# Kernel optimization log

Measured on AMD Instinct MI355X. Metric: run time of the kernel, lower is better.

## Reference

```python
import jax, jax.numpy as jnp
import numpy as np

N_NODES = 50000
N_EDGES = 800000
N_GRAPHS = 256
F_IN = 112   # num_features
DIM = 32     # hidden dim of 2nd GIN layer
OUT_DIM = 64 # output_dim
BN_EPS = 1e-5


def setup_inputs() -> dict:
    key = jax.random.key(0)
    ks = jax.random.split(key, 20)
    def w(k, shape, s=0.05):
        return jax.random.normal(k, shape, dtype=jnp.float32) * s
    return {
        "x": jax.random.normal(ks[0], (N_NODES, F_IN), dtype=jnp.float32),
        "src": jax.random.randint(ks[1], (N_EDGES,), 0, N_NODES),
        "dst": jax.random.randint(ks[2], (N_EDGES,), 0, N_NODES),
        "batch": jnp.sort(jax.random.randint(ks[3], (N_NODES,), 0, N_GRAPHS)),
        # GIN layer 1 MLP: Linear(112,112) -> ReLU -> Linear(112,112)
        "g1_w1": w(ks[4], (F_IN, F_IN)), "g1_b1": jnp.zeros((F_IN,), jnp.float32),
        "g1_w2": w(ks[5], (F_IN, F_IN)), "g1_b2": jnp.zeros((F_IN,), jnp.float32),
        "bn1_g": jnp.ones((F_IN,), jnp.float32), "bn1_b": jnp.zeros((F_IN,), jnp.float32),
        # GIN layer 2 MLP: Linear(112,32) -> ReLU -> Linear(32,32)
        "g2_w1": w(ks[6], (F_IN, DIM)), "g2_b1": jnp.zeros((DIM,), jnp.float32),
        "g2_w2": w(ks[7], (DIM, DIM)), "g2_b2": jnp.zeros((DIM,), jnp.float32),
        "bn2_g": jnp.ones((DIM,), jnp.float32), "bn2_b": jnp.zeros((DIM,), jnp.float32),
        # graph-level head
        "fcxd_w": w(ks[8], (DIM, OUT_DIM)), "fcxd_b": jnp.zeros((OUT_DIM,), jnp.float32),
        "fc1_w": w(ks[9], (64, 32)), "fc1_b": jnp.zeros((32,), jnp.float32),
        "fc2_w": w(ks[10], (32, 16)), "fc2_b": jnp.zeros((16,), jnp.float32),
        "fc3_w": w(ks[11], (16, 8)), "fc3_b": jnp.zeros((8,), jnp.float32),
        "fc4_w": w(ks[12], (8, 2)), "fc4_b": jnp.zeros((2,), jnp.float32),
        "fc5_w": w(ks[13], (2, 1)), "fc5_b": jnp.zeros((1,), jnp.float32),
    }


def _batchnorm(h, g, b):
    # training-mode BatchNorm1d: batch statistics over node axis
    m = h.mean(axis=0)
    v = h.var(axis=0)
    return (h - m) * jax.lax.rsqrt(v + BN_EPS) * g + b


def reference(x, src, dst, batch,
              g1_w1, g1_b1, g1_w2, g1_b2, bn1_g, bn1_b,
              g2_w1, g2_b1, g2_w2, g2_b2, bn2_g, bn2_b,
              fcxd_w, fcxd_b, fc1_w, fc1_b, fc2_w, fc2_b,
              fc3_w, fc3_b, fc4_w, fc4_b, fc5_w, fc5_b):
    # --- GIN layer 1: agg = sum_{j in N(i)} x_j ; h = MLP(x + agg) (eps=0) ---
    agg = jax.ops.segment_sum(x[src], dst, num_segments=N_NODES)
    h = x + agg
    h = jnp.maximum(h @ g1_w1 + g1_b1, 0.0) @ g1_w2 + g1_b2
    h = jnp.maximum(h, 0.0)                     # F.relu after conv
    h = _batchnorm(h, bn1_g, bn1_b)
    # --- GIN layer 2 ---
    agg = jax.ops.segment_sum(h[src], dst, num_segments=N_NODES)
    h = h + agg
    h = jnp.maximum(h @ g2_w1 + g2_b1, 0.0) @ g2_w2 + g2_b2
    h = jnp.maximum(h, 0.0)
    h = _batchnorm(h, bn2_g, bn2_b)
    # --- global_add_pool over graph ids ---
    pooled = jax.ops.segment_sum(h, batch, num_segments=N_GRAPHS)  # [G, 32]
    z = jnp.maximum(pooled @ fcxd_w + fcxd_b, 0.0)  # dropout = identity (eval)
    # dense head: NO activations between fc1..fc5 in the original code
    z = z @ fc1_w + fc1_b
    z = z @ fc2_w + fc2_b
    z = z @ fc3_w + fc3_b
    z = z @ fc4_w + fc4_b
    z = z @ fc5_w + fc5_b
    return z  # [N_GRAPHS, 1]
```

## Files before the change

### kernel.cpp

```cpp
#include <hip/hip_runtime.h>
#include <hip/hip_fp16.h>

#define N_NODES 50000
#define N_EDGES 800000
#define N_GRAPHS 256
#define F_IN 112
#define DIM 32
#define BN_EPS 1e-5
#define HROW 128
#define CAP 64
#define CB 391
#define CBCAP 2560
#define CHUNK 8192
#define NPART 98

typedef __attribute__((ext_vector_type(8))) _Float16 half8;
typedef __attribute__((ext_vector_type(4))) float float4v;

__device__ inline unsigned short f2h_u(float f) {
    union { __half h; unsigned short u; } v; v.h = __float2half(f); return v.u;
}
__device__ inline float h2f_u(unsigned short u) {
    union { unsigned short u; __half h; } v; v.u = u; return __half2float(v.h);
}

__device__ inline void w_split_body(const float* __restrict__ W, int K, int N, int Kpad,
                                    unsigned short* __restrict__ hi_t,
                                    unsigned short* __restrict__ lo_t, int idx) {
    if (idx >= N * Kpad) return;
    int n = idx / Kpad, k = idx - n * Kpad;
    float v = (k < K) ? W[(size_t)k * N + n] : 0.f;
    unsigned short h = f2h_u(v);
    hi_t[idx] = h;
    lo_t[idx] = f2h_u(v - h2f_u(h));
}

#define MB_P  NPART
#define MB_XH (MB_P + 3125)
#define MB_W1 (MB_XH + 14)
#define MB_W2 (MB_W1 + 14)
#define MB_W4 (MB_W2 + 1)
#define MB_GB (MB_W4 + 49)
__global__ __launch_bounds__(1024) void build_kernel(
        const int* __restrict__ src, const int* __restrict__ dst,
        int* __restrict__ gcur,
        int* __restrict__ bucket,
        const float* __restrict__ X, __half* __restrict__ Xh,
        const float* __restrict__ g1_w1, unsigned short* w1h, unsigned short* w1l,
        const float* __restrict__ g1_w2, unsigned short* w2h, unsigned short* w2l,
        const float* __restrict__ g2_w2, unsigned short* w4h, unsigned short* w4l,
        const int* __restrict__ batch, int* __restrict__ goff) {
    int b = blockIdx.x;
    int t = threadIdx.x;
    if (b < MB_P) {
        __shared__ int hist[512];
        __shared__ int lofs[512];
        __shared__ int lcur[512];
        __shared__ int gbase[512];
        __shared__ int staging[CHUNK];
        int base = b * CHUNK;
        int total = min(CHUNK, N_EDGES - base);
        for (int i = t; i < 512; i += 1024) hist[i] = 0;
        __syncthreads();
        int d[8], s[8];
#pragma unroll
        for (int j = 0; j < 8; j++) {
            int i = base + j * 1024 + t;
            if (i < N_EDGES) {
                d[j] = __builtin_nontemporal_load(dst + i);
                s[j] = __builtin_nontemporal_load(src + i);
            } else {
                d[j] = -1;
            }
        }
#pragma unroll
        for (int j = 0; j < 8; j++) {
            if (d[j] >= 0) atomicAdd(&hist[d[j] >> 7], 1);
        }
        __syncthreads();
        if (t < 512) lofs[t] = hist[t];
        __syncthreads();
        for (int o = 1; o < 512; o <<= 1) {
            int add = (t < 512 && t >= o) ? lofs[t - o] : 0;
            __syncthreads();
            if (t < 512) lofs[t] += add;
            __syncthreads();
        }
        if (t < CB) {
            gbase[t] = (hist[t] > 0) ? atomicAdd(&gcur[t], hist[t]) : 0;
        }
        if (t < 512) lcur[t] = lofs[t] - hist[t];
        __syncthreads();
#pragma unroll
        for (int j = 0; j < 8; j++) {
            if (d[j] >= 0) {
                int bb = d[j] >> 7;
                int p = atomicAdd(&lcur[bb], 1);
                staging[p] = (d[j] << 16) | s[j];
            }
        }
        __syncthreads();
        for (int p = t; p < total; p += 1024) {
            int e = staging[p];
            int bb = ((unsigned)e >> 16) >> 7;
            int ls = lofs[bb] - hist[bb];
            int di = gbase[bb] + (p - ls);
            if (di < CBCAP) bucket[(size_t)bb * CBCAP + di] = e;
        }
    } else if (b < MB_XH) {
        int idx = (b - MB_P) * 1024 + t;
        if (idx >= N_NODES * (HROW / 2)) return;
        int row = idx / (HROW / 2), c2 = idx - row * (HROW / 2);
        int col = c2 * 2;
        float2 v = make_float2(0.f, 0.f);
        if (col < F_IN) v = *(const float2*)(X + (size_t)row * F_IN + col);
        ((__half2*)Xh)[idx] = __floats2half2_rn(v.x, v.y);
    } else if (b < MB_W1) {
        w_split_body(g1_w1, F_IN, F_IN, 128, w1h, w1l, (b - MB_XH) * 1024 + t);
    } else if (b < MB_W2) {
        w_split_body(g1_w2, F_IN, F_IN, 128, w2h, w2l, (b - MB_W1) * 1024 + t);
    } else if (b < MB_W4) {
        w_split_body(g2_w2, DIM, DIM, 32, w4h, w4l, (b - MB_W2) * 1024 + t);
    } else {
        int i = (b - MB_W4) * 1024 + t;
        if (i >= N_NODES) return;
        int cur = batch[i];
        int prev = (i == 0) ? -1 : batch[i - 1];
        for (int g = prev + 1; g <= cur; g++) goff[g] = i;
        if (i == N_NODES - 1) {
            for (int g = cur + 1; g <= N_GRAPHS; g++) goff[g] = N_NODES;
        }
    }
}

__global__ __launch_bounds__(1024) void bin_build(const int* __restrict__ gcur,
                                                  const int* __restrict__ bucket,
                                                  unsigned short* __restrict__ perm_pad,
                                                  int* __restrict__ deg) {
    __shared__ __align__(16) unsigned short bins[128][CAP];
    __shared__ int lcur[128];
    int b = blockIdx.x, t = threadIdx.x;
    if (t < 128) lcur[t] = 0;
    __syncthreads();
    int count = min(gcur[b], CBCAP);
    for (int i = t; i < count; i += 1024) {
        int e = bucket[(size_t)b * CBCAP + i];
        int l = ((unsigned)e >> 16) & 127;
        int s = e & 0xFFFF;
        int c = atomicAdd(&lcur[l], 1);
        if (c < CAP) bins[l][c] = (unsigned short)s;
    }
    __syncthreads();
    if (t < 128) {
        int node = b * 128 + t;
        if (node < N_NODES) deg[node] = min(lcur[t], CAP);
    }
    for (int i = t; i < 128 * (CAP / 8); i += 1024) {
        int l = i >> 3, q = i & 7;
        int node = b * 128 + l;
        if (node < N_NODES) {
            ((int4*)&perm_pad[(size_t)node * CAP])[q] = ((const int4*)bins[l])[q];
        }
    }
}

__global__ __launch_bounds__(256) void agg_kernel(const float* __restrict__ X,
                                                  const __half* __restrict__ Xh,
                                                  const int* __restrict__ deg_arr,
                                                  const unsigned short* __restrict__ perm_pad,
                                                  __half* __restrict__ out, int M) {
    constexpr int P = F_IN / 2;
    int w = (blockIdx.x * 256 + threadIdx.x) >> 6;
    int lane = threadIdx.x & 63;
    if (w >= M) return;
    int deg = deg_arr[w];
    const unsigned short* pl = perm_pad + (size_t)w * CAP;
    float ax = 0.f, ay = 0.f;
    int e = 0;
    for (; e + 16 <= deg; e += 16) {
        int s[16];
#pragma unroll
        for (int j = 0; j < 16; j++) s[j] = pl[e + j];
        float2 v[16];
#pragma unroll
        for (int j = 0; j < 16; j++)
            v[j] = __half22float2(*(const __half2*)(Xh + (size_t)s[j] * HROW + 2 * lane));
#pragma unroll
        for (int j = 0; j < 16; j++) { ax += v[j].x; ay += v[j].y; }
    }
    for (; e + 4 <= deg; e += 4) {
        int s0 = pl[e], s1 = pl[e + 1], s2 = pl[e + 2], s3 = pl[e + 3];
        float2 v0 = __half22float2(*(const __half2*)(Xh + (size_t)s0 * HROW + 2 * lane));
        float2 v1 = __half22float2(*(const __half2*)(Xh + (size_t)s1 * HROW + 2 * lane));
        float2 v2 = __half22float2(*(const __half2*)(Xh + (size_t)s2 * HROW + 2 * lane));
        float2 v3 = __half22float2(*(const __half2*)(Xh + (size_t)s3 * HROW + 2 * lane));
        ax += (v0.x + v1.x) + (v2.x + v3.x);
        ay += (v0.y + v1.y) + (v2.y + v3.y);
    }
    for (; e < deg; e++) {
        int s = pl[e];
        float2 v = __half22float2(*(const __half2*)(Xh + (size_t)s * HROW + 2 * lane));
        ax += v.x;
        ay += v.y;
    }
    float2 self = make_float2(0.f, 0.f);
    if (lane < P) self = *(const float2*)(X + (size_t)w * F_IN + 2 * lane);
    ((__half2*)(out + (size_t)w * HROW))[lane] = __floats2half2_rn(self.x + ax, self.y + ay);
}

__global__ __launch_bounds__(256) void agg32_kernel(const __half* __restrict__ Y,
                                                    const int* __restrict__ deg_arr,
                                                    const unsigned short* __restrict__ perm_pad,
                                                    const float* __restrict__ c0,
                                                    const float* __restrict__ b1,
                                                    __half* __restrict__ out, int M) {
    int w = (blockIdx.x * 256 + threadIdx.x) >> 6;
    int lane = threadIdx.x & 63;
    if (w >= M) return;
    int f = lane & 15;
    int g = lane >> 4;
    int deg = deg_arr[w];
    const unsigned short* pl = perm_pad + (size_t)w * CAP;
    float ax = 0.f, ay = 0.f;
    int e = g;
    for (; e + 4 < deg; e += 8) {
        int s0 = pl[e], s1 = pl[e + 4];
        float2 v0 = __half22float2(*(const __half2*)(Y + (size_t)s0 * DIM + 2 * f));
        float2 v1 = __half22float2(*(const __half2*)(Y + (size_t)s1 * DIM + 2 * f));
        ax += v0.x + v1.x;
        ay += v0.y + v1.y;
    }
    if (e < deg) {
        int s0 = pl[e];
        float2 v0 = __half22float2(*(const __half2*)(Y + (size_t)s0 * DIM + 2 * f));
        ax += v0.x;
        ay += v0.y;
    }
    ax += __shfl_xor(ax, 16); ax += __shfl_xor(ax, 32);
    ay += __shfl_xor(ay, 16); ay += __shfl_xor(ay, 32);
    if (g == 0) {
        float2 self = __half22float2(*(const __half2*)(Y + (size_t)w * DIM + 2 * f));
        float deg1 = (float)(deg + 1);
        float zx = fmaxf(self.x + ax + deg1 * c0[2 * f] + b1[2 * f], 0.f);
        float zy = fmaxf(self.y + ay + deg1 * c0[2 * f + 1] + b1[2 * f + 1], 0.f);
        ((__half2*)(out + (size_t)w * DIM))[f] = __floats2half2_rn(zx, zy);
    }
}

__global__ __launch_bounds__(256) void w3_fold(const float* __restrict__ W,
                                               const float* __restrict__ s1,
                                               const float* __restrict__ t1,
                                               unsigned short* __restrict__ hi_t,
                                               unsigned short* __restrict__ lo_t,
                                               float* __restrict__ c0) {
    int idx = blockIdx.x * 256 + threadIdx.x;
    if (idx < DIM * 128) {
        int n = idx >> 7, k = idx & 127;
        float v = (k < F_IN) ? s1[k] * W[(size_t)k * DIM + n] : 0.f;
        unsigned short h = f2h_u(v);
        hi_t[idx] = h;
        lo_t[idx] = f2h_u(v - h2f_u(h));
    }
    if (blockIdx.x == 0 && threadIdx.x < DIM) {
        int n = threadIdx.x;
        float acc = 0.f;
        for (int k = 0; k < F_IN; k++) acc += t1[k] * W[(size_t)k * DIM + n];
        c0[n] = acc;
    }
}

__global__ __launch_bounds__(256) void gemm_mlp112(const unsigned short* __restrict__ A,
                                                   const unsigned short* __restrict__ W1h,
                                                   const unsigned short* __restrict__ W1l,
                                                   const float* __restrict__ b1,
                                                   const unsigned short* __restrict__ W2h,
                                                   const unsigned short* __restrict__ W2l,
                                                   const float* __restrict__ b2,
                                                   __half* __restrict__ Ch,
                                                   float* __restrict__ pbuf, int M) {
    constexpr int NT = 7, N = 112, Kpad = 128, TS = 136;
    __shared__ __align__(16) char smem[64 * TS * 2 + 2 * N * 32 * 2 + 64 * 32 * 2];
    unsigned short* T1 = (unsigned short*)smem;
    unsigned short* Wh = (unsigned short*)(smem + 64 * TS * 2);
    unsigned short* Wl = Wh + N * 32;
    unsigned short* Ah = Wl + N * 32;
    float* sls = (float*)Ah;
    int t = threadIdx.x;
    int lane = t & 63, wid = t >> 6;
    int r0 = blockIdx.x * 64;
    int m = lane & 15, quad = lane >> 4;

    for (int i = t; i < 64 * 16; i += 256) {
        T1[(i >> 4) * TS + 112 + (i & 15)] = 0;
    }

    float4v acc[NT];
#pragma unroll
    for (int nt = 0; nt < NT; nt++) acc[nt] = (float4v){0.f, 0.f, 0.f, 0.f};

    for (int c = 0; c < 4; c++) {
        int kc = c * 32;
        {
            int row = t >> 2, seg = t & 3;
            int grow = r0 + row;
            uint4 v = make_uint4(0, 0, 0, 0);
            if (grow < M) v = *(const uint4*)(A + (size_t)grow * HROW + kc + seg * 8);
            *(uint4*)&Ah[row * 32 + seg * 8] = v;
        }
        for (int idx = t; idx < N * 8; idx += 256) {
            int n = idx >> 3, w = idx & 7;
            int gsrc = n * (Kpad / 4) + (kc >> 2) + w;
            ((uint2*)Wh)[idx] = ((const uint2*)W1h)[gsrc];
            ((uint2*)Wl)[idx] = ((const uint2*)W1l)[gsrc];
        }
        __syncthreads();
        half8 a = *(const half8*)&Ah[(wid * 16 + m) * 32 + quad * 8];
#pragma unroll
        for (int nt = 0; nt < NT; nt++) {
            half8 b_h = *(const half8*)&Wh[(nt * 16 + m) * 32 + quad * 8];
            half8 b_l = *(const half8*)&Wl[(nt * 16 + m) * 32 + quad * 8];
            acc[nt] = __builtin_amdgcn_mfma_f32_16x16x32_f16(a, b_h, acc[nt], 0, 0, 0);
            acc[nt] = __builtin_amdgcn_mfma_f32_16x16x32_f16(a, b_l, acc[nt], 0, 0, 0);
        }
        __syncthreads();
    }

#pragma unroll
    for (int nt = 0; nt < NT; nt++) {
        int col = nt * 16 + m;
        float bb = b1[col];
#pragma unroll
        for (int r = 0; r < 4; r++) {
            int row = wid * 16 + quad * 4 + r;
            T1[row * TS + col] = f2h_u(fmaxf(acc[nt][r] + bb, 0.f));
        }
        acc[nt] = (float4v){0.f, 0.f, 0.f, 0.f};
    }
    __syncthreads();

    for (int c = 0; c < 4; c++) {
        int kc = c * 32;
        for (int idx = t; idx < N * 8; idx += 256) {
            int n = idx >> 3, w = idx & 7;
            int gsrc = n * (Kpad / 4) + (kc >> 2) + w;
            ((uint2*)Wh)[idx] = ((const uint2*)W2h)[gsrc];
            ((uint2*)Wl)[idx] = ((const uint2*)W2l)[gsrc];
        }
        __syncthreads();
        half8 a = *(const half8*)&T1[(wid * 16 + m) * TS + kc + quad * 8];
#pragma unroll
        for (int nt = 0; nt < NT; nt++) {
            half8 b_h = *(const half8*)&Wh[(nt * 16 + m) * 32 + quad * 8];
            half8 b_l = *(const half8*)&Wl[(nt * 16 + m) * 32 + quad * 8];
            acc[nt] = __builtin_amdgcn_mfma_f32_16x16x32_f16(a, b_h, acc[nt], 0, 0, 0);
            acc[nt] = __builtin_amdgcn_mfma_f32_16x16x32_f16(a, b_l, acc[nt], 0, 0, 0);
        }
        __syncthreads();
    }

    float st_s[NT], st_q[NT];
#pragma unroll
    for (int nt = 0; nt < NT; nt++) {
        int col = nt * 16 + m;
        float bb = b2[col];
        float s_loc = 0.f, q_loc = 0.f;
#pragma unroll
        for (int r = 0; r < 4; r++) {
            int row = r0 + wid * 16 + quad * 4 + r;
            float v = fmaxf(acc[nt][r] + bb, 0.f);
            if (row < M) {
                Ch[(size_t)row * HROW + col] = __float2half(v);
                s_loc += v;
                q_loc += v * v;
            }
        }
        st_s[nt] = s_loc;
        st_q[nt] = q_loc;
    }
    for (int i = t; i < 64 * 2; i += 256) {
        int row = r0 + (i >> 1), o = (i & 1) * 8;
        if (row < M) *(uint4*)((unsigned short*)Ch + (size_t)row * HROW + 112 + o) = make_uint4(0, 0, 0, 0);
    }
#pragma unroll
    for (int nt = 0; nt < NT; nt++) {
        float s = st_s[nt], q = st_q[nt];
        s += __shfl_xor(s, 16); s += __shfl_xor(s, 32);
        q += __shfl_xor(q, 16); q += __shfl_xor(q, 32);
        if (quad == 0) {
            sls[wid * 2 * N + nt * 16 + m] = s;
            sls[wid * 2 * N + N + nt * 16 + m] = q;
        }
    }
    __syncthreads();
    for (int j = t; j < 2 * N; j += 256) {
        pbuf[(size_t)blockIdx.x * 2 * N + j] = sls[0 * 2 * N + j] + sls[1 * 2 * N + j] +
                                               sls[2 * 2 * N + j] + sls[3 * 2 * N + j];
    }
}

template <int NT, int KC, int AS, bool RELU, int CHS, bool STATS>
__global__ __launch_bounds__(256) void gemm_mfma_h(const unsigned short* __restrict__ A,
                                                   const unsigned short* __restrict__ Whi,
                                                   const unsigned short* __restrict__ Wlo,
                                                   const float* __restrict__ bias,
                                                   float* __restrict__ C,
                                                   __half* __restrict__ Ch,
                                                   float* __restrict__ pbuf, int M) {
    constexpr int N = NT * 16;
    constexpr int Kpad = KC * 32;
    __shared__ __align__(16) unsigned short Ah[64 * 32];
    __shared__ __align__(16) unsigned short Wh[N * 32];
    __shared__ __align__(16) unsigned short Wl[N * 32];
    int t = threadIdx.x;
    int lane = t & 63, wid = t >> 6;
    int r0 = blockIdx.x * 64;
    int m = lane & 15, quad = lane >> 4;

    float4v acc[NT];
#pragma unroll
    for (int nt = 0; nt < NT; nt++) acc[nt] = (float4v){0.f, 0.f, 0.f, 0.f};

    for (int c = 0; c < KC; c++) {
        int kc = c * 32;
        {
            int row = t >> 2, seg = t & 3;
            int grow = r0 + row;
            uint4 v = make_uint4(0, 0, 0, 0);
            if (grow < M) v = *(const uint4*)(A + (size_t)grow * AS + kc + seg * 8);
            *(uint4*)&Ah[row * 32 + seg * 8] = v;
        }
        for (int idx = t; idx < N * 8; idx += 256) {
            int n = idx >> 3, w = idx & 7;
            int gsrc = n * (Kpad / 4) + (kc >> 2) + w;
            ((uint2*)Wh)[idx] = ((const uint2*)Whi)[gsrc];
            ((uint2*)Wl)[idx] = ((const uint2*)Wlo)[gsrc];
        }
        __syncthreads();
        half8 a = *(const half8*)&Ah[(wid * 16 + m) * 32 + quad * 8];
#pragma unroll
        for (int nt = 0; nt < NT; nt++) {
            half8 b_h = *(const half8*)&Wh[(nt * 16 + m) * 32 + quad * 8];
            half8 b_l = *(const half8*)&Wl[(nt * 16 + m) * 32 + quad * 8];
            acc[nt] = __builtin_amdgcn_mfma_f32_16x16x32_f16(a, b_h, acc[nt], 0, 0, 0);
            acc[nt] = __builtin_amdgcn_mfma_f32_16x16x32_f16(a, b_l, acc[nt], 0, 0, 0);
        }
        __syncthreads();
    }
    float st_s[NT], st_q[NT];
#pragma unroll
    for (int nt = 0; nt < NT; nt++) {
        int col = nt * 16 + m;
        float b = bias ? bias[col] : 0.f;
        float s_loc = 0.f, q_loc = 0.f;
#pragma unroll
        for (int r = 0; r < 4; r++) {
            int row = r0 + wid * 16 + quad * 4 + r;
            float v = acc[nt][r] + b;
            if (RELU) v = fmaxf(v, 0.f);
            if (row < M) {
                if (C) C[(size_t)row * N + col] = v;
                if (Ch) Ch[(size_t)row * CHS + col] = __float2half(v);
                if (STATS) { s_loc += v; q_loc += v * v; }
            }
        }
        st_s[nt] = s_loc;
        st_q[nt] = q_loc;
    }
    if constexpr (STATS) {
        __shared__ float sls[4][2 * N];
#pragma unroll
        for (int nt = 0; nt < NT; nt++) {
            float s = st_s[nt], q = st_q[nt];
            s += __shfl_xor(s, 16); s += __shfl_xor(s, 32);
            q += __shfl_xor(q, 16); q += __shfl_xor(q, 32);
            if (quad == 0) {
                sls[wid][nt * 16 + m] = s;
                sls[wid][N + nt * 16 + m] = q;
            }
        }
        __syncthreads();
        for (int j = t; j < 2 * N; j += 256) {
            pbuf[(size_t)blockIdx.x * 2 * N + j] = sls[0][j] + sls[1][j] + sls[2][j] + sls[3][j];
        }
    }
}

template <int F, int BLOCKS>
__global__ __launch_bounds__(256) void bn_finalize_par(const float* __restrict__ pbuf,
                                                       const float* __restrict__ g,
                                                       const float* __restrict__ b,
                                                       float* __restrict__ s,
                                                       float* __restrict__ tt, int M) {
    __shared__ double red[256];
    int j = blockIdx.x;
    int t = threadIdx.x;
    double sum = 0.0, sq = 0.0;
    for (int i = t; i < BLOCKS; i += 256) {
        sum += (double)pbuf[(size_t)i * 2 * F + j];
        sq  += (double)pbuf[(size_t)i * 2 * F + F + j];
    }
    red[t] = sum;
    __syncthreads();
    for (int o = 128; o > 0; o >>= 1) { if (t < o) red[t] += red[t + o]; __syncthreads(); }
    double total_sum = red[0];
    __syncthreads();
    red[t] = sq;
    __syncthreads();
    for (int o = 128; o > 0; o >>= 1) { if (t < o) red[t] += red[t + o]; __syncthreads(); }
    if (t == 0) {
        double mean = total_sum / M;
        double var = red[0] / M - mean * mean;
        double sc = (double)g[j] / sqrt(var + BN_EPS);
        s[j] = (float)sc;
        tt[j] = (float)((double)b[j] - mean * sc);
    }
}

__global__ __launch_bounds__(256) void pool_head(const float* __restrict__ H2, const int* __restrict__ goff,
                                                 const float* __restrict__ s2, const float* __restrict__ t2,
                                                 const float* __restrict__ fcxd_w, const float* __restrict__ fcxd_b,
                                                 const float* __restrict__ fc1_w, const float* __restrict__ fc1_b,
                                                 const float* __restrict__ fc2_w, const float* __restrict__ fc2_b,
                                                 const float* __restrict__ fc3_w, const float* __restrict__ fc3_b,
                                                 const float* __restrict__ fc4_w, const float* __restrict__ fc4_b,
                                                 const float* __restrict__ fc5_w, const float* __restrict__ fc5_b,
                                                 float* __restrict__ out) {
    __shared__ float red[256];
    __shared__ float p[64];
    __shared__ float z[64];
    int g = blockIdx.x, t = threadIdx.x;
    int r0 = goff[g], r1 = goff[g + 1];
    int cnt = r1 - r0;
    int j = t & 31, rr = t >> 5;
    float a = 0.f;
    for (int r = r0 + rr; r < r1; r += 8) a += H2[(size_t)r * DIM + j];
    red[t] = a;
    __syncthreads();
    if (t < 32) {
        float ssum = 0.f;
        for (int q = 0; q < 8; q++) ssum += red[q * 32 + j];
        p[j] = s2[j] * ssum + (float)cnt * t2[j];
    }
    __syncthreads();
    if (t < 64) {
        float acc = fcxd_b[t];
        for (int i = 0; i < 32; i++) acc += p[i] * fcxd_w[i * 64 + t];
        z[t] = fmaxf(acc, 0.f);
    }
    __syncthreads();
    if (t < 32) {
        float acc = fc1_b[t];
        for (int i = 0; i < 64; i++) acc += z[i] * fc1_w[i * 32 + t];
        p[t] = acc;
    }
    __syncthreads();
    if (t < 16) {
        float acc = fc2_b[t];
        for (int i = 0; i < 32; i++) acc += p[i] * fc2_w[i * 16 + t];
        z[t] = acc;
    }
    __syncthreads();
    if (t < 8) {
        float acc = fc3_b[t];
        for (int i = 0; i < 16; i++) acc += z[i] * fc3_w[i * 8 + t];
        p[t] = acc;
    }
    __syncthreads();
    if (t < 2) {
        float acc = fc4_b[t];
        for (int i = 0; i < 8; i++) acc += p[i] * fc4_w[i * 2 + t];
        z[t] = acc;
    }
    __syncthreads();
    if (t == 0) {
        out[g] = z[0] * fc5_w[0] + z[1] * fc5_w[1] + fc5_b[0];
    }
}

extern "C" void kernel_launch(void* const* d_in, const int* in_sizes, int n_in,
                              void* d_out, int out_size, void* d_ws, size_t ws_size,
                              hipStream_t stream) {
    const float* x     = (const float*)d_in[0];
    const int*   src   = (const int*)d_in[1];
    const int*   dst   = (const int*)d_in[2];
    const int*   batch = (const int*)d_in[3];
    const float* g1_w1 = (const float*)d_in[4];
    const float* g1_b1 = (const float*)d_in[5];
    const float* g1_w2 = (const float*)d_in[6];
    const float* g1_b2 = (const float*)d_in[7];
    const float* bn1_g = (const float*)d_in[8];
    const float* bn1_b = (const float*)d_in[9];
    const float* g2_w1 = (const float*)d_in[10];
    const float* g2_b1 = (const float*)d_in[11];
    const float* g2_w2 = (const float*)d_in[12];
    const float* g2_b2 = (const float*)d_in[13];
    const float* bn2_g = (const float*)d_in[14];
    const float* bn2_b = (const float*)d_in[15];
    const float* fcxd_w = (const float*)d_in[16];
    const float* fcxd_b = (const float*)d_in[17];
    const float* fc1_w = (const float*)d_in[18];
    const float* fc1_b = (const float*)d_in[19];
    const float* fc2_w = (const float*)d_in[20];
    const float* fc2_b = (const float*)d_in[21];
    const float* fc3_w = (const float*)d_in[22];
    const float* fc3_b = (const float*)d_in[23];
    const float* fc4_w = (const float*)d_in[24];
    const float* fc4_b = (const float*)d_in[25];
    const float* fc5_w = (const float*)d_in[26];
    const float* fc5_b = (const float*)d_in[27];
    float* out = (float*)d_out;
    char* ws = (char*)d_ws;

    const int GEMM_MB = (N_NODES + 63) / 64;

    size_t off = 0;
    auto take = [&](size_t bytes) { size_t o = off; off += (bytes + 255) & ~(size_t)255; return o; };
    int* gcur      = (int*)(ws + take((size_t)CB * 4));
    size_t zero_bytes = off;
    int* bucket    = (int*)(ws + take((size_t)CB * CBCAP * 4));
    unsigned short* perm_pad = (unsigned short*)(ws + take((size_t)N_NODES * CAP * 2));
    int* deg       = (int*)(ws + take((size_t)N_NODES * 4));
    int* goff      = (int*)(ws + take((size_t)(N_GRAPHS + 4) * 4));
    float* s1      = (float*)(ws + take(F_IN * 4));
    float* t1      = (float*)(ws + take(F_IN * 4));
    float* s2      = (float*)(ws + take(DIM * 4));
    float* t2      = (float*)(ws + take(DIM * 4));
    float* c0      = (float*)(ws + take(DIM * 4));
    float* pb1     = (float*)(ws + take((size_t)GEMM_MB * 2 * F_IN * 4));
    float* pb2     = (float*)(ws + take((size_t)GEMM_MB * 2 * DIM * 4));
    unsigned short* w1h = (unsigned short*)(ws + take((size_t)F_IN * 128 * 2));
    unsigned short* w1l = (unsigned short*)(ws + take((size_t)F_IN * 128 * 2));
    unsigned short* w2h = (unsigned short*)(ws + take((size_t)F_IN * 128 * 2));
    unsigned short* w2l = (unsigned short*)(ws + take((size_t)F_IN * 128 * 2));
    unsigned short* w3h = (unsigned short*)(ws + take((size_t)DIM * 128 * 2));
    unsigned short* w3l = (unsigned short*)(ws + take((size_t)DIM * 128 * 2));
    unsigned short* w4h = (unsigned short*)(ws + take((size_t)DIM * 32 * 2));
    unsigned short* w4l = (unsigned short*)(ws + take((size_t)DIM * 32 * 2));
    __half* x_half = (__half*)(ws + take((size_t)N_NODES * HROW * 2));
    __half* aggA   = (__half*)(ws + take((size_t)N_NODES * HROW * 2));
    __half* h1h    = (__half*)(ws + take((size_t)N_NODES * HROW * 2));
    __half* y_half = (__half*)(ws + take((size_t)N_NODES * DIM * 2));
    __half* s1h    = (__half*)(ws + take((size_t)N_NODES * DIM * 2));
    float* bufS2   = (float*)(ws + take((size_t)N_NODES * DIM * 4));
    (void)ws_size; (void)in_sizes; (void)n_in; (void)out_size;

    hipMemsetAsync(ws, 0, zero_bytes, stream);

    build_kernel<<<MB_GB, 1024, 0, stream>>>(src, dst, gcur, bucket,
                                             x, x_half,
                                             g1_w1, w1h, w1l, g1_w2, w2h, w2l, g2_w2, w4h, w4l,
                                             batch, goff);
    bin_build<<<CB, 1024, 0, stream>>>(gcur, bucket, perm_pad, deg);

    const int AGG_BLOCKS = (N_NODES + 3) / 4;

    agg_kernel<<<AGG_BLOCKS, 256, 0, stream>>>(x, x_half, deg, perm_pad, aggA, N_NODES);
    gemm_mlp112<<<GEMM_MB, 256, 0, stream>>>((const unsigned short*)aggA, w1h, w1l, g1_b1,
                                             w2h, w2l, g1_b2, h1h, pb1, N_NODES);
    bn_finalize_par<F_IN, 782><<<F_IN, 256, 0, stream>>>(pb1, bn1_g, bn1_b, s1, t1, N_NODES);

    w3_fold<<<(DIM * 128 + 255) / 256, 256, 0, stream>>>(g2_w1, s1, t1, w3h, w3l, c0);
    gemm_mfma_h<2, 4, HROW, false, DIM, false><<<GEMM_MB, 256, 0, stream>>>(
        (const unsigned short*)h1h, w3h, w3l, nullptr, nullptr, y_half, nullptr, N_NODES);
    agg32_kernel<<<AGG_BLOCKS, 256, 0, stream>>>(y_half, deg, perm_pad, c0, g2_b1, s1h, N_NODES);
    gemm_mfma_h<2, 1, DIM, true, 0, true><<<GEMM_MB, 256, 0, stream>>>(
        (const unsigned short*)s1h, w4h, w4l, g2_b2, bufS2, nullptr, pb2, N_NODES);
    bn_finalize_par<DIM, 782><<<DIM, 256, 0, stream>>>(pb2, bn2_g, bn2_b, s2, t2, N_NODES);

    pool_head<<<N_GRAPHS, 256, 0, stream>>>(bufS2, goff, s2, t2,
                                            fcxd_w, fcxd_b, fc1_w, fc1_b, fc2_w, fc2_b,
                                            fc3_w, fc3_b, fc4_w, fc4_b, fc5_w, fc5_b, out);
}
```

Baseline: 244.9 us.

## Fuse neighbor aggregation into GIN MLP GEMMs and merge BN1 finalize with W3 fold

The layer-1 gather-sum is folded into the MLP GEMM kernel, which now writes the aggregated tile straight into shared memory instead of a global fp16 buffer. The layer-2 aggregation and ReLU are likewise fused with the second small GEMM and its BN statistics. The BN1 finalize and the W3 scale/fold are merged into one kernel that updates c0 with atomics, and c0/w3 are added to the zeroed workspace region. This drops two intermediate global round-trips and several launches. The cost is that the gather phase now runs at GEMM-grid occupancy, with 64 rows per block and higher shared-memory use, which may hide latency less well than the old standalone aggregation kernels.

```diff
diff --git a/kernel.cpp b/kernel.cpp
--- a/kernel.cpp
+++ b/kernel.cpp
@@ -13,6 +13,7 @@
 #define CBCAP 2560
 #define CHUNK 8192
 #define NPART 98
+#define GEMM_MB 782
 
 typedef __attribute__((ext_vector_type(8))) _Float16 half8;
 typedef __attribute__((ext_vector_type(4))) float float4v;
@@ -164,132 +165,75 @@
     }
 }
 
-__global__ __launch_bounds__(256) void agg_kernel(const float* __restrict__ X,
-                                                  const __half* __restrict__ Xh,
-                                                  const int* __restrict__ deg_arr,
-                                                  const unsigned short* __restrict__ perm_pad,
-                                                  __half* __restrict__ out, int M) {
-    constexpr int P = F_IN / 2;
-    int w = (blockIdx.x * 256 + threadIdx.x) >> 6;
-    int lane = threadIdx.x & 63;
-    if (w >= M) return;
-    int deg = deg_arr[w];
-    const unsigned short* pl = perm_pad + (size_t)w * CAP;
-    float ax = 0.f, ay = 0.f;
-    int e = 0;
-    for (; e + 16 <= deg; e += 16) {
-        int s[16];
-#pragma unroll
-        for (int j = 0; j < 16; j++) s[j] = pl[e + j];
-        float2 v[16];
-#pragma unroll
-        for (int j = 0; j < 16; j++)
-            v[j] = __half22float2(*(const __half2*)(Xh + (size_t)s[j] * HROW + 2 * lane));
-#pragma unroll
-        for (int j = 0; j < 16; j++) { ax += v[j].x; ay += v[j].y; }
-    }
-    for (; e + 4 <= deg; e += 4) {
-        int s0 = pl[e], s1 = pl[e + 1], s2 = pl[e + 2], s3 = pl[e + 3];
-        float2 v0 = __half22float2(*(const __half2*)(Xh + (size_t)s0 * HROW + 2 * lane));
-        float2 v1 = __half22float2(*(const __half2*)(Xh + (size_t)s1 * HROW + 2 * lane));
-        float2 v2 = __half22float2(*(const __half2*)(Xh + (size_t)s2 * HROW + 2 * lane));
-        float2 v3 = __half22float2(*(const __half2*)(Xh + (size_t)s3 * HROW + 2 * lane));
-        ax += (v0.x + v1.x) + (v2.x + v3.x);
-        ay += (v0.y + v1.y) + (v2.y + v3.y);
-    }
-    for (; e < deg; e++) {
-        int s = pl[e];
-        float2 v = __half22float2(*(const __half2*)(Xh + (size_t)s * HROW + 2 * lane));
-        ax += v.x;
-        ay += v.y;
-    }
-    float2 self = make_float2(0.f, 0.f);
-    if (lane < P) self = *(const float2*)(X + (size_t)w * F_IN + 2 * lane);
-    ((__half2*)(out + (size_t)w * HROW))[lane] = __floats2half2_rn(self.x + ax, self.y + ay);
-}
-
-__global__ __launch_bounds__(256) void agg32_kernel(const __half* __restrict__ Y,
-                                                    const int* __restrict__ deg_arr,
-                                                    const unsigned short* __restrict__ perm_pad,
-                                                    const float* __restrict__ c0,
-                                                    const float* __restrict__ b1,
-                                                    __half* __restrict__ out, int M) {
-    int w = (blockIdx.x * 256 + threadIdx.x) >> 6;
-    int lane = threadIdx.x & 63;
-    if (w >= M) return;
-    int f = lane & 15;
-    int g = lane >> 4;
-    int deg = deg_arr[w];
-    const unsigned short* pl = perm_pad + (size_t)w * CAP;
-    float ax = 0.f, ay = 0.f;
-    int e = g;
-    for (; e + 4 < deg; e += 8) {
-        int s0 = pl[e], s1 = pl[e + 4];
-        float2 v0 = __half22float2(*(const __half2*)(Y + (size_t)s0 * DIM + 2 * f));
-        float2 v1 = __half22float2(*(const __half2*)(Y + (size_t)s1 * DIM + 2 * f));
-        ax += v0.x + v1.x;
-        ay += v0.y + v1.y;
-    }
-    if (e < deg) {
-        int s0 = pl[e];
-        float2 v0 = __half22float2(*(const __half2*)(Y + (size_t)s0 * DIM + 2 * f));
-        ax += v0.x;
-        ay += v0.y;
-    }
-    ax += __shfl_xor(ax, 16); ax += __shfl_xor(ax, 32);
-    ay += __shfl_xor(ay, 16); ay += __shfl_xor(ay, 32);
-    if (g == 0) {
-        float2 self = __half22float2(*(const __half2*)(Y + (size_t)w * DIM + 2 * f));
-        float deg1 = (float)(deg + 1);
-        float zx = fmaxf(self.x + ax + deg1 * c0[2 * f] + b1[2 * f], 0.f);
-        float zy = fmaxf(self.y + ay + deg1 * c0[2 * f + 1] + b1[2 * f + 1], 0.f);
-        ((__half2*)(out + (size_t)w * DIM))[f] = __floats2half2_rn(zx, zy);
-    }
-}
-
-__global__ __launch_bounds__(256) void w3_fold(const float* __restrict__ W,
-                                               const float* __restrict__ s1,
-                                               const float* __restrict__ t1,
-                                               unsigned short* __restrict__ hi_t,
-                                               unsigned short* __restrict__ lo_t,
-                                               float* __restrict__ c0) {
-    int idx = blockIdx.x * 256 + threadIdx.x;
-    if (idx < DIM * 128) {
-        int n = idx >> 7, k = idx & 127;
-        float v = (k < F_IN) ? s1[k] * W[(size_t)k * DIM + n] : 0.f;
-        unsigned short h = f2h_u(v);
-        hi_t[idx] = h;
-        lo_t[idx] = f2h_u(v - h2f_u(h));
-    }
-    if (blockIdx.x == 0 && threadIdx.x < DIM) {
-        int n = threadIdx.x;
-        float acc = 0.f;
-        for (int k = 0; k < F_IN; k++) acc += t1[k] * W[(size_t)k * DIM + n];
-        c0[n] = acc;
-    }
-}
-
-__global__ __launch_bounds__(256) void gemm_mlp112(const unsigned short* __restrict__ A,
-                                                   const unsigned short* __restrict__ W1h,
-                                                   const unsigned short* __restrict__ W1l,
-                                                   const float* __restrict__ b1,
-                                                   const unsigned short* __restrict__ W2h,
-                                                   const unsigned short* __restrict__ W2l,
-                                                   const float* __restrict__ b2,
-                                                   __half* __restrict__ Ch,
-                                                   float* __restrict__ pbuf, int M) {
-    constexpr int NT = 7, N = 112, Kpad = 128, TS = 136;
-    __shared__ __align__(16) char smem[64 * TS * 2 + 2 * N * 32 * 2 + 64 * 32 * 2];
-    unsigned short* T1 = (unsigned short*)smem;
-    unsigned short* Wh = (unsigned short*)(smem + 64 * TS * 2);
-    unsigned short* Wl = Wh + N * 32;
-    unsigned short* Ah = Wl + N * 32;
-    float* sls = (float*)Ah;
+__global__ __launch_bounds__(256) void gin1_fused(const float* __restrict__ X,
+        const __half* __restrict__ Xh,
+        const int* __restrict__ deg_arr,
+        const unsigned short* __restrict__ perm_pad,
+        const unsigned short* __restrict__ W1h, const unsigned short* __restrict__ W1l,
+        const float* __restrict__ b1,
+        const unsigned short* __restrict__ W2h, const unsigned short* __restrict__ W2l,
+        const float* __restrict__ b2,
+        __half* __restrict__ Ch, float* __restrict__ pbuf, int M) {
+    constexpr int NT = 7, N = 112, Kpad = 128, TS = 136, AS = 136;
+    __shared__ __align__(16) unsigned short Afull[64 * AS];
+    __shared__ __align__(16) unsigned short T1[64 * TS];
+    __shared__ __align__(16) unsigned short Wh[N * 32];
+    __shared__ __align__(16) unsigned short Wl[N * 32];
+    float* sls = (float*)Afull;
     int t = threadIdx.x;
     int lane = t & 63, wid = t >> 6;
     int r0 = blockIdx.x * 64;
     int m = lane & 15, quad = lane >> 4;
 
+    for (int idx = t; idx < N * 8; idx += 256) {
+        int n = idx >> 3, w = idx & 7;
+        int gsrc = n * (Kpad / 4) + w;
+        ((uint2*)Wh)[idx] = ((const uint2*)W1h)[gsrc];
+        ((uint2*)Wl)[idx] = ((const uint2*)W1l)[gsrc];
+    }
+
+    for (int i = 0; i < 16; i++) {
+        int row = wid * 16 + i;
+        int grow = r0 + row;
+        float ax = 0.f, ay = 0.f;
+        if (grow < M) {
+            int deg = deg_arr[grow];
+            const unsigned short* pl = perm_pad + (size_t)grow * CAP;
+            int e = 0;
+            for (; e + 16 <= deg; e += 16) {
+                int s[16];
+#pragma unroll
+                for (int j = 0; j < 16; j++) s[j] = pl[e + j];
+                float2 v[16];
+#pragma unroll
+                for (int j = 0; j < 16; j++)
+                    v[j] = __half22float2(*(const __half2*)(Xh + (size_t)s[j] * HROW + 2 * lane));
+#pragma unroll
+                for (int j = 0; j < 16; j++) { ax += v[j].x; ay += v[j].y; }
+            }
+            for (; e + 4 <= deg; e += 4) {
+                int s0 = pl[e], s1 = pl[e + 1], s2 = pl[e + 2], s3 = pl[e + 3];
+                float2 v0 = __half22float2(*(const __half2*)(Xh + (size_t)s0 * HROW + 2 * lane));
+                float2 v1 = __half22float2(*(const __half2*)(Xh + (size_t)s1 * HROW + 2 * lane));
+                float2 v2 = __half22float2(*(const __half2*)(Xh + (size_t)s2 * HROW + 2 * lane));
+                float2 v3 = __half22float2(*(const __half2*)(Xh + (size_t)s3 * HROW + 2 * lane));
+                ax += (v0.x + v1.x) + (v2.x + v3.x);
+                ay += (v0.y + v1.y) + (v2.y + v3.y);
+            }
+            for (; e < deg; e++) {
+                int s = pl[e];
+                float2 v = __half22float2(*(const __half2*)(Xh + (size_t)s * HROW + 2 * lane));
+                ax += v.x;
+                ay += v.y;
+            }
+            if (lane < F_IN / 2) {
+                float2 self = *(const float2*)(X + (size_t)grow * F_IN + 2 * lane);
+                ax += self.x;
+                ay += self.y;
+            }
+        }
+        ((__half2*)&Afull[row * AS])[lane] = __floats2half2_rn(ax, ay);
+    }
     for (int i = t; i < 64 * 16; i += 256) {
         T1[(i >> 4) * TS + 112 + (i & 15)] = 0;
     }
@@ -300,21 +244,16 @@
 
     for (int c = 0; c < 4; c++) {
         int kc = c * 32;
-        {
-            int row = t >> 2, seg = t & 3;
-            int grow = r0 + row;
-            uint4 v = make_uint4(0, 0, 0, 0);
-            if (grow < M) v = *(const uint4*)(A + (size_t)grow * HROW + kc + seg * 8);
-            *(uint4*)&Ah[row * 32 + seg * 8] = v;
-        }
-        for (int idx = t; idx < N * 8; idx += 256) {
-            int n = idx >> 3, w = idx & 7;
-            int gsrc = n * (Kpad / 4) + (kc >> 2) + w;
-            ((uint2*)Wh)[idx] = ((const uint2*)W1h)[gsrc];
-            ((uint2*)Wl)[idx] = ((const uint2*)W1l)[gsrc];
-        }
-        __syncthreads();
-        half8 a = *(const half8*)&Ah[(wid * 16 + m) * 32 + quad * 8];
+        if (c > 0) {
+            for (int idx = t; idx < N * 8; idx += 256) {
+                int n = idx >> 3, w = idx & 7;
+                int gsrc = n * (Kpad / 4) + (kc >> 2) + w;
+                ((uint2*)Wh)[idx] = ((const uint2*)W1h)[gsrc];
+                ((uint2*)Wl)[idx] = ((const uint2*)W1l)[gsrc];
+            }
+        }
+        __syncthreads();
+        half8 a = *(const half8*)&Afull[(wid * 16 + m) * AS + kc + quad * 8];
 #pragma unroll
         for (int nt = 0; nt < NT; nt++) {
             half8 b_h = *(const half8*)&Wh[(nt * 16 + m) * 32 + quad * 8];
@@ -395,6 +334,48 @@
     for (int j = t; j < 2 * N; j += 256) {
         pbuf[(size_t)blockIdx.x * 2 * N + j] = sls[0 * 2 * N + j] + sls[1 * 2 * N + j] +
                                                sls[2 * 2 * N + j] + sls[3 * 2 * N + j];
+    }
+}
+
+__global__ __launch_bounds__(256) void bn1_w3(const float* __restrict__ pbuf,
+                                              const float* __restrict__ gg,
+                                              const float* __restrict__ bb,
+                                              const float* __restrict__ W,
+                                              unsigned short* __restrict__ w3h,
+                                              unsigned short* __restrict__ w3l,
+                                              float* __restrict__ c0, int M) {
+    __shared__ double red[256];
+    __shared__ float sv[2];
+    int j = blockIdx.x;
+    int t = threadIdx.x;
+    double sum = 0.0, sq = 0.0;
+    for (int i = t; i < GEMM_MB; i += 256) {
+        sum += (double)pbuf[(size_t)i * 2 * F_IN + j];
+        sq  += (double)pbuf[(size_t)i * 2 * F_IN + F_IN + j];
+    }
+    red[t] = sum;
+    __syncthreads();
+    for (int o = 128; o > 0; o >>= 1) { if (t < o) red[t] += red[t + o]; __syncthreads(); }
+    double total_sum = red[0];
+    __syncthreads();
+    red[t] = sq;
+    __syncthreads();
+    for (int o = 128; o > 0; o >>= 1) { if (t < o) red[t] += red[t + o]; __syncthreads(); }
+    if (t == 0) {
+        double mean = total_sum / M;
+        double var = red[0] / M - mean * mean;
+        double sc = (double)gg[j] / sqrt(var + BN_EPS);
+        sv[0] = (float)sc;
+        sv[1] = (float)((double)bb[j] - mean * sc);
+    }
+    __syncthreads();
+    if (t < DIM) {
+        float w = W[(size_t)j * DIM + t];
+        float v = sv[0] * w;
+        unsigned short h = f2h_u(v);
+        w3h[t * 128 + j] = h;
+        w3l[t * 128 + j] = f2h_u(v - h2f_u(h));
+        atomicAdd(&c0[t], sv[1] * w);
     }
 }
 
@@ -482,6 +463,117 @@
         for (int j = t; j < 2 * N; j += 256) {
             pbuf[(size_t)blockIdx.x * 2 * N + j] = sls[0][j] + sls[1][j] + sls[2][j] + sls[3][j];
         }
+    }
+}
+
+__global__ __launch_bounds__(256) void gin2_fused(const __half* __restrict__ Y,
+        const int* __restrict__ deg_arr,
+        const unsigned short* __restrict__ perm_pad,
+        const float* __restrict__ c0, const float* __restrict__ cb1,
+        const unsigned short* __restrict__ W4h, const unsigned short* __restrict__ W4l,
+        const float* __restrict__ bias,
+        float* __restrict__ C, float* __restrict__ pbuf, int M) {
+    constexpr int NT = 2, N = 32;
+    __shared__ __align__(16) unsigned short As[64 * 32];
+    __shared__ __align__(16) unsigned short Wh[N * 32];
+    __shared__ __align__(16) unsigned short Wl[N * 32];
+    __shared__ float sls[4][2 * N];
+    int t = threadIdx.x;
+    int lane = t & 63, wid = t >> 6;
+    int r0 = blockIdx.x * 64;
+    int m = lane & 15, quad = lane >> 4;
+    int f = m, g = quad;
+
+    for (int idx = t; idx < N * 8; idx += 256) {
+        int n = idx >> 3, w = idx & 7;
+        int gsrc = n * 8 + w;
+        ((uint2*)Wh)[idx] = ((const uint2*)W4h)[gsrc];
+        ((uint2*)Wl)[idx] = ((const uint2*)W4l)[gsrc];
+    }
+
+    for (int i = 0; i < 16; i++) {
+        int row = wid * 16 + i;
+        int grow = r0 + row;
+        float ax = 0.f, ay = 0.f;
+        int deg = 0;
+        if (grow < M) {
+            deg = deg_arr[grow];
+            const unsigned short* pl = perm_pad + (size_t)grow * CAP;
+            int e = g;
+            for (; e + 4 < deg; e += 8) {
+                int s0 = pl[e], s1 = pl[e + 4];
+                float2 v0 = __half22float2(*(const __half2*)(Y + (size_t)s0 * DIM + 2 * f));
+                float2 v1 = __half22float2(*(const __half2*)(Y + (size_t)s1 * DIM + 2 * f));
+                ax += v0.x + v1.x;
+                ay += v0.y + v1.y;
+            }
+            if (e < deg) {
+                int s0 = pl[e];
+                float2 v0 = __half22float2(*(const __half2*)(Y + (size_t)s0 * DIM + 2 * f));
+                ax += v0.x;
+                ay += v0.y;
+            }
+        }
+        ax += __shfl_xor(ax, 16); ax += __shfl_xor(ax, 32);
+        ay += __shfl_xor(ay, 16); ay += __shfl_xor(ay, 32);
+        if (g == 0) {
+            __half2 hv = __floats2half2_rn(0.f, 0.f);
+            if (grow < M) {
+                float2 self = __half22float2(*(const __half2*)(Y + (size_t)grow * DIM + 2 * f));
+                float deg1 = (float)(deg + 1);
+                float zx = fmaxf(self.x + ax + deg1 * c0[2 * f] + cb1[2 * f], 0.f);
+                float zy = fmaxf(self.y + ay + deg1 * c0[2 * f + 1] + cb1[2 * f + 1], 0.f);
+                hv = __floats2half2_rn(zx, zy);
+            }
+            ((__half2*)&As[row * 32])[f] = hv;
+        }
+    }
+    __syncthreads();
+
+    float4v acc[NT];
+#pragma unroll
+    for (int nt = 0; nt < NT; nt++) acc[nt] = (float4v){0.f, 0.f, 0.f, 0.f};
+    half8 a = *(const half8*)&As[(wid * 16 + m) * 32 + quad * 8];
+#pragma unroll
+    for (int nt = 0; nt < NT; nt++) {
+        half8 b_h = *(const half8*)&Wh[(nt * 16 + m) * 32 + quad * 8];
+        half8 b_l = *(const half8*)&Wl[(nt * 16 + m) * 32 + quad * 8];
+        acc[nt] = __builtin_amdgcn_mfma_f32_16x16x32_f16(a, b_h, acc[nt], 0, 0, 0);
+        acc[nt] = __builtin_amdgcn_mfma_f32_16x16x32_f16(a, b_l, acc[nt], 0, 0, 0);
+    }
+
+    float st_s[NT], st_q[NT];
+#pragma unroll
+    for (int nt = 0; nt < NT; nt++) {
+        int col = nt * 16 + m;
+        float b = bias[col];
+        float s_loc = 0.f, q_loc = 0.f;
+#pragma unroll
+        for (int r = 0; r < 4; r++) {
+            int row = r0 + wid * 16 + quad * 4 + r;
+            float v = fmaxf(acc[nt][r] + b, 0.f);
+            if (row < M) {
+                C[(size_t)row * N + col] = v;
+                s_loc += v;
+                q_loc += v * v;
+            }
+        }
+        st_s[nt] = s_loc;
+        st_q[nt] = q_loc;
+    }
+#pragma unroll
+    for (int nt = 0; nt < NT; nt++) {
+        float s = st_s[nt], q = st_q[nt];
+        s += __shfl_xor(s, 16); s += __shfl_xor(s, 32);
+        q += __shfl_xor(q, 16); q += __shfl_xor(q, 32);
+        if (quad == 0) {
+            sls[wid][nt * 16 + m] = s;
+            sls[wid][N + nt * 16 + m] = q;
+        }
+    }
+    __syncthreads();
+    for (int j = t; j < 2 * N; j += 256) {
+        pbuf[(size_t)blockIdx.x * 2 * N + j] = sls[0][j] + sls[1][j] + sls[2][j] + sls[3][j];
     }
 }
 
@@ -611,36 +703,30 @@
     float* out = (float*)d_out;
     char* ws = (char*)d_ws;
 
-    const int GEMM_MB = (N_NODES + 63) / 64;
-
     size_t off = 0;
     auto take = [&](size_t bytes) { size_t o = off; off += (bytes + 255) & ~(size_t)255; return o; };
     int* gcur      = (int*)(ws + take((size_t)CB * 4));
+    float* c0      = (float*)(ws + take(DIM * 4));
+    unsigned short* w3h = (unsigned short*)(ws + take((size_t)DIM * 128 * 2));
+    unsigned short* w3l = (unsigned short*)(ws + take((size_t)DIM * 128 * 2));
     size_t zero_bytes = off;
     int* bucket    = (int*)(ws + take((size_t)CB * CBCAP * 4));
     unsigned short* perm_pad = (unsigned short*)(ws + take((size_t)N_NODES * CAP * 2));
     int* deg       = (int*)(ws + take((size_t)N_NODES * 4));
     int* goff      = (int*)(ws + take((size_t)(N_GRAPHS + 4) * 4));
-    float* s1      = (float*)(ws + take(F_IN * 4));
-    float* t1      = (float*)(ws + take(F_IN * 4));
     float* s2      = (float*)(ws + take(DIM * 4));
     float* t2      = (float*)(ws + take(DIM * 4));
-    float* c0      = (float*)(ws + take(DIM * 4));
     float* pb1     = (float*)(ws + take((size_t)GEMM_MB * 2 * F_IN * 4));
     float* pb2     = (float*)(ws + take((size_t)GEMM_MB * 2 * DIM * 4));
     unsigned short* w1h = (unsigned short*)(ws + take((size_t)F_IN * 128 * 2));
     unsigned short* w1l = (unsigned short*)(ws + take((size_t)F_IN * 128 * 2));
     unsigned short* w2h = (unsigned short*)(ws + take((size_t)F_IN * 128 * 2));
     unsigned short* w2l = (unsigned short*)(ws + take((size_t)F_IN * 128 * 2));
-    unsigned short* w3h = (unsigned short*)(ws + take((size_t)DIM * 128 * 2));
-    unsigned short* w3l = (unsigned short*)(ws + take((size_t)DIM * 128 * 2));
     unsigned short* w4h = (unsigned short*)(ws + take((size_t)DIM * 32 * 2));
     unsigned short* w4l = (unsigned short*)(ws + take((size_t)DIM * 32 * 2));
     __half* x_half = (__half*)(ws + take((size_t)N_NODES * HROW * 2));
-    __half* aggA   = (__half*)(ws + take((size_t)N_NODES * HROW * 2));
     __half* h1h    = (__half*)(ws + take((size_t)N_NODES * HROW * 2));
     __half* y_half = (__half*)(ws + take((size_t)N_NODES * DIM * 2));
-    __half* s1h    = (__half*)(ws + take((size_t)N_NODES * DIM * 2));
     float* bufS2   = (float*)(ws + take((size_t)N_NODES * DIM * 4));
     (void)ws_size; (void)in_sizes; (void)n_in; (void)out_size;
 
@@ -652,20 +738,16 @@
                                              batch, goff);
     bin_build<<<CB, 1024, 0, stream>>>(gcur, bucket, perm_pad, deg);
 
-    const int AGG_BLOCKS = (N_NODES + 3) / 4;
-
-    agg_kernel<<<AGG_BLOCKS, 256, 0, stream>>>(x, x_half, deg, perm_pad, aggA, N_NODES);
-    gemm_mlp112<<<GEMM_MB, 256, 0, stream>>>((const unsigned short*)aggA, w1h, w1l, g1_b1,
-                                             w2h, w2l, g1_b2, h1h, pb1, N_NODES);
-    bn_finalize_par<F_IN, 782><<<F_IN, 256, 0, stream>>>(pb1, bn1_g, bn1_b, s1, t1, N_NODES);
-
-    w3_fold<<<(DIM * 128 + 255) / 256, 256, 0, stream>>>(g2_w1, s1, t1, w3h, w3l, c0);
+    gin1_fused<<<GEMM_MB, 256, 0, stream>>>(x, x_half, deg, perm_pad,
+                                            w1h, w1l, g1_b1, w2h, w2l, g1_b2,
+                                            h1h, pb1, N_NODES);
+    bn1_w3<<<F_IN, 256, 0, stream>>>(pb1, bn1_g, bn1_b, g2_w1, w3h, w3l, c0, N_NODES);
+
     gemm_mfma_h<2, 4, HROW, false, DIM, false><<<GEMM_MB, 256, 0, stream>>>(
         (const unsigned short*)h1h, w3h, w3l, nullptr, nullptr, y_half, nullptr, N_NODES);
-    agg32_kernel<<<AGG_BLOCKS, 256, 0, stream>>>(y_half, deg, perm_pad, c0, g2_b1, s1h, N_NODES);
-    gemm_mfma_h<2, 1, DIM, true, 0, true><<<GEMM_MB, 256, 0, stream>>>(
-        (const unsigned short*)s1h, w4h, w4l, g2_b2, bufS2, nullptr, pb2, N_NODES);
-    bn_finalize_par<DIM, 782><<<DIM, 256, 0, stream>>>(pb2, bn2_g, bn2_b, s2, t2, N_NODES);
+    gin2_fused<<<GEMM_MB, 256, 0, stream>>>(y_half, deg, perm_pad, c0, g2_b1,
+                                            w4h, w4l, g2_b2, bufS2, pb2, N_NODES);
+    bn_finalize_par<DIM, GEMM_MB><<<DIM, 256, 0, stream>>>(pb2, bn2_g, bn2_b, s2, t2, N_NODES);
 
     pool_head<<<N_GRAPHS, 256, 0, stream>>>(bufS2, goff, s2, t2,
                                             fcxd_w, fcxd_b, fc1_w, fc1_b, fc2_w, fc2_b,
```

Result: slower. 322.1 us (+31.5%).
